# Performance work log

Measured on AMD Instinct MI355X. Metric: run time of the kernel, lower is better.

The kernel has to match this reference:

```python
import jax, jax.numpy as jnp
import numpy as np

N_USERS = 100000
N_ITEMS = 50000
D = 64
N_LAYERS = 3
E_RAW = 2_000_000
B = 4096


def setup_inputs() -> dict:
    rng = np.random.RandomState(0)
    u = rng.randint(0, N_USERS, E_RAW).astype(np.int64)
    i = rng.randint(0, N_ITEMS, E_RAW).astype(np.int64)
    lin = np.unique(u * N_ITEMS + i)  # dedupe interactions like the dok_matrix would
    u = (lin // N_ITEMS).astype(np.int32)
    i = (lin % N_ITEMS).astype(np.int32)
    deg_u = np.bincount(u, minlength=N_USERS).astype(np.float64)
    deg_i = np.bincount(i, minlength=N_ITEMS).astype(np.float64)
    inv_u = np.where(deg_u > 0, 1.0 / np.sqrt(np.maximum(deg_u, 1.0)), 0.0)
    inv_i = np.where(deg_i > 0, 1.0 / np.sqrt(np.maximum(deg_i, 1.0)), 0.0)
    val = (inv_u[u] * inv_i[i]).astype(np.float32)  # D^-1/2 A D^-1/2 entries
    # symmetric bipartite Laplacian: user block rows then item block rows
    rows = np.concatenate([u, i + N_USERS]).astype(np.int32)
    cols = np.concatenate([i + N_USERS, u]).astype(np.int32)
    vals = np.concatenate([val, val])

    key = jax.random.key(0)
    k1, k2, k3, k4 = jax.random.split(key, 4)
    embeds = jax.random.normal(k1, (N_USERS + N_ITEMS, D), jnp.float32) * 0.1
    users = jax.random.randint(k2, (B,), 0, N_USERS)
    pos_items = jax.random.randint(k3, (B,), 0, N_ITEMS)
    neg_items = jax.random.randint(k4, (B,), 0, N_ITEMS)
    return dict(embeds=embeds, vals=jnp.asarray(vals), rows=jnp.asarray(rows),
                cols=jnp.asarray(cols), users=users, pos_items=pos_items,
                neg_items=neg_items)


def reference(embeds, vals, rows, cols, users, pos_items, neg_items):
    N = N_USERS + N_ITEMS
    cur = embeds
    acc = embeds  # running sum over layer embeddings (incl. layer 0)
    for _ in range(N_LAYERS):
        msg = vals[:, None] * cur[cols]                      # [nnz, D] gather
        cur = jax.ops.segment_sum(msg, rows, num_segments=N)  # SpMM scatter-add
        acc = acc + cur
    mean = acc / (N_LAYERS + 1)
    user_e = mean[:N_USERS]
    item_e = mean[N_USERS:]
    return user_e[users], item_e[pos_items], item_e[neg_items]
```

## Files before the change

kernel.cpp:

```cpp
#include <hip/hip_runtime.h>
#include <hip/hip_bf16.h>

#define N_USERS 100000
#define N_ITEMS 50000
#define N_TOT   150000
#define D       64
#define NBUCK   ((N_ITEMS + 127) >> 7)
#define BCAP    6144

typedef float v2f __attribute__((ext_vector_type(2)));

__device__ __forceinline__ unsigned bf16rn(float f) {
    unsigned x = __float_as_uint(f);
    return (x + 0x7FFFu + ((x >> 16) & 1u)) >> 16;
}
__device__ __forceinline__ unsigned packbf(float a, float b) {
    return bf16rn(a) | (bf16rn(b) << 16);
}


#define BS_B 391
__global__ __launch_bounds__(256) void pre_misc_kernel(
        const int* __restrict__ rows, int* __restrict__ user_ptr, int E,
        const int* __restrict__ users, const int* __restrict__ pos,
        const int* __restrict__ neg, unsigned char* __restrict__ flags, int B) {
    int b = blockIdx.x, t = threadIdx.x;
    if (b < BS_B) {
        int r = b * 256 + t;
        if (r <= N_USERS) {
            int lo = 0, hi = E;
            while (lo < hi) {
                int mid = (lo + hi) >> 1;
                if (rows[mid] < r) lo = mid + 1; else hi = mid;
            }
            user_ptr[r] = lo;
        }
    } else {
        int k = (b - BS_B) * 256 + t;
        if (k < 3 * B) {
            int row;
            if (k < B)          row = users[k];
            else if (k < 2 * B) row = N_USERS + pos[k - B];
            else                row = N_USERS + neg[k - 2 * B];
            flags[row] = 1;
        }
    }
}

__global__ __launch_bounds__(256) void coarse_scatter_kernel(
        const int* __restrict__ rows, const int* __restrict__ cols,
        int* __restrict__ ccur, int* __restrict__ tmp,
        unsigned short* __restrict__ cols16, int E) {
    __shared__ int cnt[NBUCK];
    __shared__ int basep[NBUCK];
    const int K = 16;
    int chunk = blockIdx.x * (256 * K);
    for (int i = threadIdx.x; i < NBUCK; i += 256) cnt[i] = 0;
    __syncthreads();
    int pk[K]; int bk[K];
    #pragma unroll
    for (int k = 0; k < K; ++k) {
        int e = chunk + k * 256 + (int)threadIdx.x;
        if (e < E) {
            int i = cols[e] - N_USERS;
            cols16[e] = (unsigned short)i;
            bk[k] = i >> 7;
            pk[k] = ((i & 127) << 17) | rows[e];
            atomicAdd(&cnt[bk[k]], 1);
        } else bk[k] = -1;
    }
    __syncthreads();
    for (int i = threadIdx.x; i < NBUCK; i += 256) {
        int c = cnt[i];
        basep[i] = c ? atomicAdd(&ccur[i], c) : 0;
        cnt[i] = 0;
    }
    __syncthreads();
    #pragma unroll
    for (int k = 0; k < K; ++k) {
        if (bk[k] >= 0) {
            int pos = basep[bk[k]] + atomicAdd(&cnt[bk[k]], 1);
            if (pos < BCAP)
                tmp[(size_t)bk[k] * BCAP + pos] = pk[k];
        }
    }
}

__global__ __launch_bounds__(256) void fine_sort_kernel(
        const int* __restrict__ tmp, const int* __restrict__ ccur,
        int* __restrict__ item_beg, int* __restrict__ item_end,
        int* __restrict__ nbr) {
    __shared__ int stage[BCAP];
    __shared__ int hist[128];
    __shared__ int scn[128];
    __shared__ int curs[128];
    int b = blockIdx.x, t = threadIdx.x;
    int n = ccur[b]; if (n > BCAP) n = BCAP;
    const int* src = tmp + (size_t)b * BCAP;
    if (t < 128) hist[t] = 0;
    __syncthreads();
    for (int p = t; p < n; p += 256) {
        int q = src[p];
        stage[p] = q;
        atomicAdd(&hist[q >> 17], 1);
    }
    __syncthreads();
    if (t < 128) scn[t] = hist[t];
    __syncthreads();
    for (int off = 1; off < 128; off <<= 1) {
        int x = (t < 128 && t >= off) ? scn[t - off] : 0;
        __syncthreads();
        if (t < 128) scn[t] += x;
        __syncthreads();
    }
    if (t < 128) {
        int excl = scn[t] - hist[t];
        curs[t] = excl;
        int gi = (b << 7) + t;
        if (gi < N_ITEMS) {
            item_beg[gi] = b * BCAP + excl;
            item_end[gi] = b * BCAP + excl + hist[t];
        }
    }
    __syncthreads();
    int* dst = nbr + (size_t)b * BCAP;
    for (int p = t; p < n; p += 256) {
        int q = stage[p];
        int pos = atomicAdd(&curs[q >> 17], 1);
        dst[pos] = q & 0x1FFFF;
    }
}

__global__ __launch_bounds__(256) void conv_scale_kernel(
        const float* __restrict__ embeds, const int* __restrict__ user_ptr,
        const int* __restrict__ item_beg, const int* __restrict__ item_end,
        unsigned* __restrict__ ebfS, unsigned* __restrict__ bb1,
        float* __restrict__ invrow) {
    int gid = blockIdx.x * blockDim.x + threadIdx.x;
    int row = gid >> 4, fl = gid & 15;
    if (row > N_TOT) return;
    if (row == N_TOT) {
        *(uint2*)(ebfS + (size_t)row * 32 + fl * 2) = make_uint2(0u, 0u);
        *(uint2*)(bb1  + (size_t)row * 32 + fl * 2) = make_uint2(0u, 0u);
        if (fl == 0) invrow[row] = 0.f;
        return;
    }
    int deg;
    if (row < N_USERS) deg = user_ptr[row + 1] - user_ptr[row];
    else { int i = row - N_USERS; deg = item_end[i] - item_beg[i]; }
    float inv = (deg > 0) ? (float)(1.0 / sqrt((double)deg)) : 0.f;
    float4 v = *(const float4*)(embeds + (size_t)row * D + fl * 4);
    uint2 o;
    o.x = packbf(inv * v.x, inv * v.y);
    o.y = packbf(inv * v.z, inv * v.w);
    *(uint2*)(ebfS + (size_t)row * 32 + fl * 2) = o;
    if (fl == 0) invrow[row] = inv;
}

__global__ __launch_bounds__(256) void agg_kernel(
        const unsigned* __restrict__ gsrc,
        float* __restrict__ nxt, unsigned* __restrict__ nxtb,
        const float* __restrict__ invrow,
        const unsigned char* __restrict__ flags,
        const int* __restrict__ user_ptr, const unsigned short* __restrict__ cols16,
        const int* __restrict__ item_beg, const int* __restrict__ item_end,
        const int* __restrict__ nbr) {
    int wave = (int)((blockIdx.x * blockDim.x + threadIdx.x) >> 6);
    int lane = (int)(threadIdx.x & 63);
    if (wave >= N_TOT) return;
    int g  = lane >> 3;
    int fl = lane & 7;

    bool is_user = wave < N_USERS;
    int s, epos;
    const unsigned* sb;
    int dummy;
    if (is_user) {
        s = user_ptr[wave]; epos = user_ptr[wave + 1];
        sb = gsrc + (size_t)N_USERS * 32; dummy = N_ITEMS;
    } else {
        int i = wave - N_USERS; s = item_beg[i]; epos = item_end[i];
        sb = gsrc; dummy = N_TOT;
    }

    v2f a0 = {0.f, 0.f}, a1 = {0.f, 0.f}, a2 = {0.f, 0.f}, a3 = {0.f, 0.f};

    for (int base = s; base < epos; base += 64) {
        int cnt = epos - base; if (cnt > 64) cnt = 64;
        int col = dummy;
        if (lane < cnt)
            col = is_user ? (int)cols16[base + lane] : nbr[base + lane];
        int tcount = (cnt + 7) >> 3;
        #pragma unroll 4
        for (int t = 0; t < tcount; ++t) {
            int c = __shfl(col, 8 * t + g);
            uint4 q = *(const uint4*)(sb + (size_t)c * 32 + fl * 4);
            v2f p0 = {__uint_as_float(q.x << 16), __uint_as_float(q.x & 0xFFFF0000u)};
            v2f p1 = {__uint_as_float(q.y << 16), __uint_as_float(q.y & 0xFFFF0000u)};
            v2f p2 = {__uint_as_float(q.z << 16), __uint_as_float(q.z & 0xFFFF0000u)};
            v2f p3 = {__uint_as_float(q.w << 16), __uint_as_float(q.w & 0xFFFF0000u)};
            a0 += p0; a1 += p1; a2 += p2; a3 += p3;
        }
    }
    float acc[8] = {a0.x, a0.y, a1.x, a1.y, a2.x, a2.y, a3.x, a3.y};
    #pragma unroll
    for (int j = 0; j < 8; ++j) {
        acc[j] += __shfl_xor(acc[j], 8);
        acc[j] += __shfl_xor(acc[j], 16);
        acc[j] += __shfl_xor(acc[j], 32);
    }
    if (lane < 8) {
        float inv = invrow[wave];
        float f[8];
        #pragma unroll
        for (int j = 0; j < 8; ++j) f[j] = inv * acc[j];
        uint4 o;
        o.x = packbf(inv * f[0], inv * f[1]); o.y = packbf(inv * f[2], inv * f[3]);
        o.z = packbf(inv * f[4], inv * f[5]); o.w = packbf(inv * f[6], inv * f[7]);
        *(uint4*)(nxtb + (size_t)wave * 32 + fl * 4) = o;
        if (flags[wave]) {
            size_t ro = (size_t)wave * D + fl * 8;
            *(float4*)(nxt + ro)     = make_float4(f[0], f[1], f[2], f[3]);
            *(float4*)(nxt + ro + 4) = make_float4(f[4], f[5], f[6], f[7]);
        }
    }
}

__global__ __launch_bounds__(256) void agg3_fused_kernel(
        const unsigned* __restrict__ gsrc,
        const float* __restrict__ e0, const float* __restrict__ e1,
        const float* __restrict__ e2, const float* __restrict__ invrow,
        const int* __restrict__ users, const int* __restrict__ pos,
        const int* __restrict__ neg,
        const int* __restrict__ user_ptr, const unsigned short* __restrict__ cols16,
        const int* __restrict__ item_beg, const int* __restrict__ item_end,
        const int* __restrict__ nbr,
        float* __restrict__ out, int B) {
    int slot = (int)((blockIdx.x * blockDim.x + threadIdx.x) >> 6);
    int lane = (int)(threadIdx.x & 63);
    if (slot >= 3 * B) return;
    int g  = lane >> 3;
    int fl = lane & 7;

    int row;
    if (slot < B)          row = users[slot];
    else if (slot < 2 * B) row = N_USERS + pos[slot - B];
    else                   row = N_USERS + neg[slot - 2 * B];

    bool is_user = row < N_USERS;
    int s, epos;
    const unsigned* sb;
    int dummy;
    if (is_user) {
        s = user_ptr[row]; epos = user_ptr[row + 1];
        sb = gsrc + (size_t)N_USERS * 32; dummy = N_ITEMS;
    } else {
        int i = row - N_USERS; s = item_beg[i]; epos = item_end[i];
        sb = gsrc; dummy = N_TOT;
    }

    v2f a0 = {0.f, 0.f}, a1 = {0.f, 0.f}, a2 = {0.f, 0.f}, a3 = {0.f, 0.f};

    for (int base = s; base < epos; base += 64) {
        int cnt = epos - base; if (cnt > 64) cnt = 64;
        int col = dummy;
        if (lane < cnt)
            col = is_user ? (int)cols16[base + lane] : nbr[base + lane];
        int tcount = (cnt + 7) >> 3;
        #pragma unroll 4
        for (int t = 0; t < tcount; ++t) {
            int c = __shfl(col, 8 * t + g);
            uint4 q = *(const uint4*)(sb + (size_t)c * 32 + fl * 4);
            v2f p0 = {__uint_as_float(q.x << 16), __uint_as_float(q.x & 0xFFFF0000u)};
            v2f p1 = {__uint_as_float(q.y << 16), __uint_as_float(q.y & 0xFFFF0000u)};
            v2f p2 = {__uint_as_float(q.z << 16), __uint_as_float(q.z & 0xFFFF0000u)};
            v2f p3 = {__uint_as_float(q.w << 16), __uint_as_float(q.w & 0xFFFF0000u)};
            a0 += p0; a1 += p1; a2 += p2; a3 += p3;
        }
    }
    float acc[8] = {a0.x, a0.y, a1.x, a1.y, a2.x, a2.y, a3.x, a3.y};
    #pragma unroll
    for (int j = 0; j < 8; ++j) {
        acc[j] += __shfl_xor(acc[j], 8);
        acc[j] += __shfl_xor(acc[j], 16);
        acc[j] += __shfl_xor(acc[j], 32);
    }
    if (lane < 8) {
        float inv = invrow[row];
        size_t ro = (size_t)row * D + fl * 8;
        float4 x0 = *(const float4*)(e0 + ro), x1 = *(const float4*)(e0 + ro + 4);
        float4 y0 = *(const float4*)(e1 + ro), y1 = *(const float4*)(e1 + ro + 4);
        float4 z0 = *(const float4*)(e2 + ro), z1 = *(const float4*)(e2 + ro + 4);
        float4 r0, r1;
        r0.x = (x0.x + y0.x + z0.x + inv * acc[0]) * 0.25f;
        r0.y = (x0.y + y0.y + z0.y + inv * acc[1]) * 0.25f;
        r0.z = (x0.z + y0.z + z0.z + inv * acc[2]) * 0.25f;
        r0.w = (x0.w + y0.w + z0.w + inv * acc[3]) * 0.25f;
        r1.x = (x1.x + y1.x + z1.x + inv * acc[4]) * 0.25f;
        r1.y = (x1.y + y1.y + z1.y + inv * acc[5]) * 0.25f;
        r1.z = (x1.z + y1.z + z1.z + inv * acc[6]) * 0.25f;
        r1.w = (x1.w + y1.w + z1.w + inv * acc[7]) * 0.25f;
        size_t oo = (size_t)slot * D + fl * 8;
        *(float4*)(out + oo)     = r0;
        *(float4*)(out + oo + 4) = r1;
    }
}

extern "C" void kernel_launch(void* const* d_in, const int* in_sizes, int n_in,
                              void* d_out, int out_size, void* d_ws, size_t ws_size,
                              hipStream_t stream) {
    const float* embeds = (const float*)d_in[0];
    const int*   rows   = (const int*)d_in[2];
    const int*   cols   = (const int*)d_in[3];
    const int*   users  = (const int*)d_in[4];
    const int*   pos    = (const int*)d_in[5];
    const int*   neg    = (const int*)d_in[6];
    const int E2 = in_sizes[1];
    const int E  = E2 / 2;
    const int B  = in_sizes[4];

    char* ws = (char*)d_ws;
    size_t off = 0;
    auto alloc = [&](size_t bytes) { void* p = ws + off; off = (off + bytes + 255) & ~(size_t)255; return p; };
    float*    buf1     = (float*)   alloc((size_t)N_TOT * D * sizeof(float));
    float*    buf2     = (float*)   alloc((size_t)N_TOT * D * sizeof(float));
    unsigned* ebfS     = (unsigned*)alloc((size_t)(N_TOT + 1) * 32 * sizeof(unsigned));
    unsigned* bb1      = (unsigned*)alloc((size_t)(N_TOT + 1) * 32 * sizeof(unsigned));
    int*      nbr      = (int*)     alloc((size_t)NBUCK * BCAP * sizeof(int));
    unsigned short* cols16 = (unsigned short*)alloc((size_t)E * sizeof(unsigned short));
    int*      user_ptr = (int*)     alloc((size_t)(N_USERS + 1) * sizeof(int));
    int*      ccur     = (int*)     alloc((size_t)NBUCK * sizeof(int));
    int*      item_beg = (int*)     alloc((size_t)N_ITEMS * sizeof(int));
    int*      item_end = (int*)     alloc((size_t)N_ITEMS * sizeof(int));
    float*    invrow   = (float*)   alloc((size_t)(N_TOT + 1) * sizeof(float));
    unsigned char* flags = (unsigned char*)alloc((size_t)N_TOT);
    int*      tmp      = (int*)buf1;

    hipMemsetAsync(ccur, 0, (size_t)NBUCK * sizeof(int), stream);
    hipMemsetAsync(flags, 0, (size_t)N_TOT, stream);
    pre_misc_kernel<<<BS_B + (3 * B + 255) / 256, 256, 0, stream>>>(
        rows, user_ptr, E, users, pos, neg, flags, B);
    coarse_scatter_kernel<<<(E + 4095) / 4096, 256, 0, stream>>>(rows, cols, ccur, tmp, cols16, E);
    fine_sort_kernel<<<NBUCK, 256, 0, stream>>>(tmp, ccur, item_beg, item_end, nbr);
    conv_scale_kernel<<<((N_TOT + 1) * 16 + 255) / 256, 256, 0, stream>>>(
        embeds, user_ptr, item_beg, item_end, ebfS, bb1, invrow);

    const int blocks = (N_TOT + 3) / 4;
    agg_kernel<<<blocks, 256, 0, stream>>>(ebfS, buf1, bb1, invrow, flags, user_ptr,
                                           cols16, item_beg, item_end, nbr);
    agg_kernel<<<blocks, 256, 0, stream>>>(bb1, buf2, ebfS, invrow, flags, user_ptr,
                                           cols16, item_beg, item_end, nbr);

    agg3_fused_kernel<<<(3 * B + 3) / 4, 256, 0, stream>>>(
        ebfS, embeds, buf1, buf2, invrow, users, pos, neg,
        user_ptr, cols16, item_beg, item_end, nbr, (float*)d_out, B);
}
```

Before: 333.1 us.

## Fuse preprocessing kernels into two launches and compute degree scaling in-place

Merges the user-pointer binary search, flag marking and coarse bucket scatter into one launch. The user-row bf16 scaled conversion moves into the same blocks that compute user_ptr, and the item conversion moves into the fine sort kernel using the histogram counts as degrees. This cuts four preprocessing launches to two and removes the separate conversion pass that re-read the degree arrays. In exchange the launches are heterogeneous, and the extra shared memory and work may lower occupancy in the sort kernel.

```diff
diff --git a/kernel.cpp b/kernel.cpp
--- a/kernel.cpp
+++ b/kernel.cpp
@@ -7,6 +7,8 @@
 #define D       64
 #define NBUCK   ((N_ITEMS + 127) >> 7)
 #define BCAP    6144
+#define CONVU_B 391
+#define FLAG_B  48
 
 typedef float v2f __attribute__((ext_vector_type(2)));
 
@@ -17,26 +19,57 @@
 __device__ __forceinline__ unsigned packbf(float a, float b) {
     return bf16rn(a) | (bf16rn(b) << 16);
 }
-
-
-#define BS_B 391
-__global__ __launch_bounds__(256) void pre_misc_kernel(
-        const int* __restrict__ rows, int* __restrict__ user_ptr, int E,
+__device__ __forceinline__ int lower_bound(const int* __restrict__ a, int n, int key) {
+    int lo = 0, hi = n;
+    while (lo < hi) {
+        int mid = (lo + hi) >> 1;
+        if (a[mid] < key) lo = mid + 1; else hi = mid;
+    }
+    return lo;
+}
+
+__global__ __launch_bounds__(256) void preA_kernel(
+        const float* __restrict__ embeds, const int* __restrict__ rows,
+        const int* __restrict__ cols, int* __restrict__ user_ptr,
+        unsigned* __restrict__ ebfS, float* __restrict__ invrow,
         const int* __restrict__ users, const int* __restrict__ pos,
-        const int* __restrict__ neg, unsigned char* __restrict__ flags, int B) {
+        const int* __restrict__ neg, unsigned char* __restrict__ flags,
+        int* __restrict__ ccur, int* __restrict__ tmp,
+        unsigned short* __restrict__ cols16, int E, int B) {
     int b = blockIdx.x, t = threadIdx.x;
-    if (b < BS_B) {
-        int r = b * 256 + t;
-        if (r <= N_USERS) {
-            int lo = 0, hi = E;
-            while (lo < hi) {
-                int mid = (lo + hi) >> 1;
-                if (rows[mid] < r) lo = mid + 1; else hi = mid;
+    if (b < CONVU_B) {
+        __shared__ int ptr_s[257];
+        __shared__ float inv_s[256];
+        int base = b * 256;
+        int r = base + t;
+        int v = lower_bound(rows, E, r);
+        ptr_s[t] = v;
+        if (r <= N_USERS) user_ptr[r] = v;
+        if (t == 0) ptr_s[256] = lower_bound(rows, E, base + 256);
+        __syncthreads();
+        if (r < N_USERS) {
+            int deg = ptr_s[t + 1] - ptr_s[t];
+            float inv = (deg > 0) ? (float)(1.0 / sqrt((double)deg)) : 0.f;
+            inv_s[t] = inv;
+            invrow[r] = inv;
+        } else inv_s[t] = 0.f;
+        __syncthreads();
+        int fl = t & 15;
+        #pragma unroll
+        for (int i = 0; i < 16; ++i) {
+            int lr = i * 16 + (t >> 4);
+            int row = base + lr;
+            if (row < N_USERS) {
+                float inv = inv_s[lr];
+                float4 v4 = *(const float4*)(embeds + (size_t)row * D + fl * 4);
+                uint2 o;
+                o.x = packbf(inv * v4.x, inv * v4.y);
+                o.y = packbf(inv * v4.z, inv * v4.w);
+                *(uint2*)(ebfS + (size_t)row * 32 + fl * 2) = o;
             }
-            user_ptr[r] = lo;
-        }
-    } else {
-        int k = (b - BS_B) * 256 + t;
+        }
+    } else if (b < CONVU_B + FLAG_B) {
+        int k = (b - CONVU_B) * 256 + t;
         if (k < 3 * B) {
             int row;
             if (k < B)          row = users[k];
@@ -44,57 +77,63 @@
             else                row = N_USERS + neg[k - 2 * B];
             flags[row] = 1;
         }
-    }
-}
-
-__global__ __launch_bounds__(256) void coarse_scatter_kernel(
-        const int* __restrict__ rows, const int* __restrict__ cols,
-        int* __restrict__ ccur, int* __restrict__ tmp,
-        unsigned short* __restrict__ cols16, int E) {
-    __shared__ int cnt[NBUCK];
-    __shared__ int basep[NBUCK];
-    const int K = 16;
-    int chunk = blockIdx.x * (256 * K);
-    for (int i = threadIdx.x; i < NBUCK; i += 256) cnt[i] = 0;
-    __syncthreads();
-    int pk[K]; int bk[K];
-    #pragma unroll
-    for (int k = 0; k < K; ++k) {
-        int e = chunk + k * 256 + (int)threadIdx.x;
-        if (e < E) {
-            int i = cols[e] - N_USERS;
-            cols16[e] = (unsigned short)i;
-            bk[k] = i >> 7;
-            pk[k] = ((i & 127) << 17) | rows[e];
-            atomicAdd(&cnt[bk[k]], 1);
-        } else bk[k] = -1;
-    }
-    __syncthreads();
-    for (int i = threadIdx.x; i < NBUCK; i += 256) {
-        int c = cnt[i];
-        basep[i] = c ? atomicAdd(&ccur[i], c) : 0;
-        cnt[i] = 0;
-    }
-    __syncthreads();
-    #pragma unroll
-    for (int k = 0; k < K; ++k) {
-        if (bk[k] >= 0) {
-            int pos = basep[bk[k]] + atomicAdd(&cnt[bk[k]], 1);
-            if (pos < BCAP)
-                tmp[(size_t)bk[k] * BCAP + pos] = pk[k];
-        }
-    }
-}
-
-__global__ __launch_bounds__(256) void fine_sort_kernel(
+    } else {
+        __shared__ int cnt[NBUCK];
+        __shared__ int basep[NBUCK];
+        const int K = 16;
+        int chunk = (b - CONVU_B - FLAG_B) * (256 * K);
+        for (int i = t; i < NBUCK; i += 256) cnt[i] = 0;
+        __syncthreads();
+        int pk[K]; int bk[K];
+        #pragma unroll
+        for (int k = 0; k < K; ++k) {
+            int e = chunk + k * 256 + t;
+            if (e < E) {
+                int i = cols[e] - N_USERS;
+                cols16[e] = (unsigned short)i;
+                bk[k] = i >> 7;
+                pk[k] = ((i & 127) << 17) | rows[e];
+                atomicAdd(&cnt[bk[k]], 1);
+            } else bk[k] = -1;
+        }
+        __syncthreads();
+        for (int i = t; i < NBUCK; i += 256) {
+            int c = cnt[i];
+            basep[i] = c ? atomicAdd(&ccur[i], c) : 0;
+            cnt[i] = 0;
+        }
+        __syncthreads();
+        #pragma unroll
+        for (int k = 0; k < K; ++k) {
+            if (bk[k] >= 0) {
+                int pos2 = basep[bk[k]] + atomicAdd(&cnt[bk[k]], 1);
+                if (pos2 < BCAP)
+                    tmp[(size_t)bk[k] * BCAP + pos2] = pk[k];
+            }
+        }
+    }
+}
+
+__global__ __launch_bounds__(256) void preB_kernel(
         const int* __restrict__ tmp, const int* __restrict__ ccur,
+        const float* __restrict__ embeds,
         int* __restrict__ item_beg, int* __restrict__ item_end,
-        int* __restrict__ nbr) {
+        int* __restrict__ nbr, unsigned* __restrict__ ebfS,
+        unsigned* __restrict__ bb1, float* __restrict__ invrow) {
+    int b = blockIdx.x, t = threadIdx.x;
+    if (b == NBUCK) {
+        if (t < 16) {
+            *(uint2*)(ebfS + (size_t)N_TOT * 32 + t * 2) = make_uint2(0u, 0u);
+            *(uint2*)(bb1  + (size_t)N_TOT * 32 + t * 2) = make_uint2(0u, 0u);
+        }
+        if (t == 0) invrow[N_TOT] = 0.f;
+        return;
+    }
     __shared__ int stage[BCAP];
     __shared__ int hist[128];
     __shared__ int scn[128];
     __shared__ int curs[128];
-    int b = blockIdx.x, t = threadIdx.x;
+    __shared__ float inv_s[128];
     int n = ccur[b]; if (n > BCAP) n = BCAP;
     const int* src = tmp + (size_t)b * BCAP;
     if (t < 128) hist[t] = 0;
@@ -117,9 +156,12 @@
         int excl = scn[t] - hist[t];
         curs[t] = excl;
         int gi = (b << 7) + t;
+        float inv = (hist[t] > 0) ? (float)(1.0 / sqrt((double)hist[t])) : 0.f;
+        inv_s[t] = inv;
         if (gi < N_ITEMS) {
             item_beg[gi] = b * BCAP + excl;
             item_end[gi] = b * BCAP + excl + hist[t];
+            invrow[N_USERS + gi] = inv;
         }
     }
     __syncthreads();
@@ -129,32 +171,21 @@
         int pos = atomicAdd(&curs[q >> 17], 1);
         dst[pos] = q & 0x1FFFF;
     }
-}
-
-__global__ __launch_bounds__(256) void conv_scale_kernel(
-        const float* __restrict__ embeds, const int* __restrict__ user_ptr,
-        const int* __restrict__ item_beg, const int* __restrict__ item_end,
-        unsigned* __restrict__ ebfS, unsigned* __restrict__ bb1,
-        float* __restrict__ invrow) {
-    int gid = blockIdx.x * blockDim.x + threadIdx.x;
-    int row = gid >> 4, fl = gid & 15;
-    if (row > N_TOT) return;
-    if (row == N_TOT) {
-        *(uint2*)(ebfS + (size_t)row * 32 + fl * 2) = make_uint2(0u, 0u);
-        *(uint2*)(bb1  + (size_t)row * 32 + fl * 2) = make_uint2(0u, 0u);
-        if (fl == 0) invrow[row] = 0.f;
-        return;
-    }
-    int deg;
-    if (row < N_USERS) deg = user_ptr[row + 1] - user_ptr[row];
-    else { int i = row - N_USERS; deg = item_end[i] - item_beg[i]; }
-    float inv = (deg > 0) ? (float)(1.0 / sqrt((double)deg)) : 0.f;
-    float4 v = *(const float4*)(embeds + (size_t)row * D + fl * 4);
-    uint2 o;
-    o.x = packbf(inv * v.x, inv * v.y);
-    o.y = packbf(inv * v.z, inv * v.w);
-    *(uint2*)(ebfS + (size_t)row * 32 + fl * 2) = o;
-    if (fl == 0) invrow[row] = inv;
+    int fl = t & 15;
+    #pragma unroll
+    for (int i = 0; i < 8; ++i) {
+        int lr = i * 16 + (t >> 4);
+        int gi = (b << 7) + lr;
+        if (gi < N_ITEMS) {
+            int row = N_USERS + gi;
+            float inv = inv_s[lr];
+            float4 v4 = *(const float4*)(embeds + (size_t)row * D + fl * 4);
+            uint2 o;
+            o.x = packbf(inv * v4.x, inv * v4.y);
+            o.y = packbf(inv * v4.z, inv * v4.w);
+            *(uint2*)(ebfS + (size_t)row * 32 + fl * 2) = o;
+        }
+    }
 }
 
 __global__ __launch_bounds__(256) void agg_kernel(
@@ -172,9 +203,8 @@
     int fl = lane & 7;
 
     bool is_user = wave < N_USERS;
-    int s, epos;
+    int s, epos, dummy;
     const unsigned* sb;
-    int dummy;
     if (is_user) {
         s = user_ptr[wave]; epos = user_ptr[wave + 1];
         sb = gsrc + (size_t)N_USERS * 32; dummy = N_ITEMS;
@@ -248,9 +278,8 @@
     else                   row = N_USERS + neg[slot - 2 * B];
 
     bool is_user = row < N_USERS;
-    int s, epos;
+    int s, epos, dummy;
     const unsigned* sb;
-    int dummy;
     if (is_user) {
         s = user_ptr[row]; epos = user_ptr[row + 1];
         sb = gsrc + (size_t)N_USERS * 32; dummy = N_ITEMS;
@@ -338,12 +367,12 @@
 
     hipMemsetAsync(ccur, 0, (size_t)NBUCK * sizeof(int), stream);
     hipMemsetAsync(flags, 0, (size_t)N_TOT, stream);
-    pre_misc_kernel<<<BS_B + (3 * B + 255) / 256, 256, 0, stream>>>(
-        rows, user_ptr, E, users, pos, neg, flags, B);
-    coarse_scatter_kernel<<<(E + 4095) / 4096, 256, 0, stream>>>(rows, cols, ccur, tmp, cols16, E);
-    fine_sort_kernel<<<NBUCK, 256, 0, stream>>>(tmp, ccur, item_beg, item_end, nbr);
-    conv_scale_kernel<<<((N_TOT + 1) * 16 + 255) / 256, 256, 0, stream>>>(
-        embeds, user_ptr, item_beg, item_end, ebfS, bb1, invrow);
+    const int scatB = (E + 4095) / 4096;
+    preA_kernel<<<CONVU_B + FLAG_B + scatB, 256, 0, stream>>>(
+        embeds, rows, cols, user_ptr, ebfS, invrow, users, pos, neg, flags,
+        ccur, tmp, cols16, E, B);
+    preB_kernel<<<NBUCK + 1, 256, 0, stream>>>(
+        tmp, ccur, embeds, item_beg, item_end, nbr, ebfS, bb1, invrow);
 
     const int blocks = (N_TOT + 3) / 4;
     agg_kernel<<<blocks, 256, 0, stream>>>(ebfS, buf1, bb1, invrow, flags, user_ptr,
```

Result: no change. 338.8 us (+1.7%).
